# Performance work log

Hardware: AMD Instinct MI355X
Metric: run time of the kernel (lower is better)

The kernel has to match this reference:

```python
import jax, jax.numpy as jnp
import numpy as np

B, L, D0, H, K = 16, 256, 64, 128, 512  # batch, seq, feat, hidden, codebook size


def _p(key, shape, scale=0.05):
    return jax.random.normal(key, shape, jnp.float32) * scale


def setup_inputs() -> dict:
    key = jax.random.key(0)
    ks = jax.random.split(key, 32)
    inp = {
        "inputs": jax.random.normal(ks[0], (B, L, D0), jnp.float32),
        "input_lens": jnp.full((B,), L, dtype=jnp.int64),
        "in_mask": jnp.ones((B, L), jnp.float32),
        # encoder params
        "enc_lin1_W": _p(ks[1], (H, D0)), "enc_lin1_b": jnp.zeros((H,), jnp.float32),
        "enc_Wih_f": _p(ks[2], (4 * H, H)), "enc_Whh_f": _p(ks[3], (4 * H, H)), "enc_b_f": jnp.zeros((4 * H,), jnp.float32),
        "enc_Wih_b": _p(ks[4], (4 * H, H)), "enc_Whh_b": _p(ks[5], (4 * H, H)), "enc_b_b": jnp.zeros((4 * H,), jnp.float32),
        "enc_lin2_W": _p(ks[6], (H, 2 * H)), "enc_lin2_b": jnp.zeros((H,), jnp.float32),
        # VQ codebook (K codes of dim H), init uniform(-1/K, 1/K) as in torch
        "vq_emb": jax.random.uniform(ks[7], (K, H), jnp.float32, -1.0 / K, 1.0 / K),
        # decoder params
        "dec_lin1_W": _p(ks[8], (H, D0)), "dec_lin1_b": jnp.zeros((H,), jnp.float32),
        "dec_Wih": _p(ks[9], (4 * H, H)), "dec_Whh": _p(ks[10], (4 * H, H)), "dec_b": jnp.zeros((4 * H,), jnp.float32),
        "attn_Wq": _p(ks[11], (H, H)), "attn_bq": jnp.zeros((H,), jnp.float32),
        "attn_Wk": _p(ks[12], (H, H)), "attn_bk": jnp.zeros((H,), jnp.float32),
        "attn_Wv": _p(ks[13], (H, H)), "attn_bv": jnp.zeros((H,), jnp.float32),
        "dec_lin2_W": _p(ks[14], (D0, H)), "dec_lin2_b": jnp.zeros((D0,), jnp.float32),
    }
    return inp


def _lstm_cell(x, h, c, Wih, Whh, b):
    g = x @ Wih.T + h @ Whh.T + b  # (B, 4H)
    i, f, gg, o = jnp.split(g, 4, axis=-1)
    c = jax.nn.sigmoid(f) * c + jax.nn.sigmoid(i) * jnp.tanh(gg)
    h = jax.nn.sigmoid(o) * jnp.tanh(c)
    return h, c


def _lstm_scan(x_blh, Wih, Whh, b, reverse=False):
    Bb = x_blh.shape[0]
    Hh = Whh.shape[1]
    init = (jnp.zeros((Bb, Hh), x_blh.dtype), jnp.zeros((Bb, Hh), x_blh.dtype))

    def step(carry, x):
        h, c = _lstm_cell(x, carry[0], carry[1], Wih, Whh, b)
        return (h, c), h

    _, hs = jax.lax.scan(step, init, jnp.swapaxes(x_blh, 0, 1), reverse=reverse)
    return jnp.swapaxes(hs, 0, 1)  # (B, L, H)


def _forward(inputs, in_mask, p):
    # ---- encoder: Linear -> ReLU -> BiLSTM -> Linear (full-length sequences) ----
    enc_x = jax.nn.relu(inputs @ p["enc_lin1_W"].T + p["enc_lin1_b"])
    hf = _lstm_scan(enc_x, p["enc_Wih_f"], p["enc_Whh_f"], p["enc_b_f"], reverse=False)
    hb = _lstm_scan(enc_x, p["enc_Wih_b"], p["enc_Whh_b"], p["enc_b_b"], reverse=True)
    ze = jnp.concatenate([hf, hb], axis=-1) @ p["enc_lin2_W"].T + p["enc_lin2_b"]  # (B,L,H)

    # ---- VQ: nearest codebook entry (expanded ||a-b||^2, avoids (B,L,K,C) tensor) ----
    emb = p["vq_emb"]  # (K, H)
    dist = (jnp.sum(ze * ze, -1, keepdims=True)
            - 2.0 * jnp.einsum("blc,kc->blk", ze, emb)
            + jnp.sum(emb * emb, -1)[None, None, :])  # (B,L,K)
    nearest = jnp.argmin(dist, axis=-1)  # (B,L) int
    zq = emb[nearest]  # (B,L,H)
    dec_in = ze + jax.lax.stop_gradient(zq - ze)  # straight-through

    k_proj = dec_in @ p["attn_Wk"].T + p["attn_bk"]  # (B,L,H)
    v_proj = dec_in @ p["attn_Wv"].T + p["attn_bv"]
    scale = 1.0 / jnp.sqrt(jnp.float32(H))
    mask_add = jnp.where(in_mask == 0, -1e9, 0.0).astype(jnp.float32)  # (B,L)

    def dec_step(carry, _):
        h, c, tok = carry
        x = jax.nn.relu(tok @ p["dec_lin1_W"].T + p["dec_lin1_b"])  # (B,H)
        h, c = _lstm_cell(x, h, c, p["dec_Wih"], p["dec_Whh"], p["dec_b"])
        q = h @ p["attn_Wq"].T + p["attn_bq"]  # (B,H)
        scores = jnp.einsum("bd,bld->bl", q, k_proj) * scale + mask_add
        attn = jax.nn.softmax(scores, axis=-1)  # (B,L)
        ctx = jnp.einsum("bl,bld->bd", attn, v_proj)  # (B,H)
        out = ctx @ p["dec_lin2_W"].T + p["dec_lin2_b"]  # (B,D0)
        return (h, c, out), (out, attn)

    Bb = inputs.shape[0]
    init = (jnp.zeros((Bb, H), jnp.float32), jnp.zeros((Bb, H), jnp.float32), jnp.zeros((Bb, D0), jnp.float32))
    _, (outs, attns) = jax.lax.scan(dec_step, init, None, length=dec_in.shape[1])
    dec_out = jnp.swapaxes(outs, 0, 1)  # (B,L,D0)
    attn_w = jnp.swapaxes(attns, 0, 1)  # (B,L,L)
    return dec_out, attn_w, ze, zq


def reference(inputs, input_lens, in_mask, enc_lin1_W, enc_lin1_b, enc_Wih_f, enc_Whh_f, enc_b_f,
              enc_Wih_b, enc_Whh_b, enc_b_b, enc_lin2_W, enc_lin2_b, vq_emb,
              dec_lin1_W, dec_lin1_b, dec_Wih, dec_Whh, dec_b,
              attn_Wq, attn_bq, attn_Wk, attn_bk, attn_Wv, attn_bv, dec_lin2_W, dec_lin2_b):
    p = dict(enc_lin1_W=enc_lin1_W, enc_lin1_b=enc_lin1_b, enc_Wih_f=enc_Wih_f, enc_Whh_f=enc_Whh_f,
             enc_b_f=enc_b_f, enc_Wih_b=enc_Wih_b, enc_Whh_b=enc_Whh_b, enc_b_b=enc_b_b,
             enc_lin2_W=enc_lin2_W, enc_lin2_b=enc_lin2_b, vq_emb=vq_emb,
             dec_lin1_W=dec_lin1_W, dec_lin1_b=dec_lin1_b, dec_Wih=dec_Wih, dec_Whh=dec_Whh, dec_b=dec_b,
             attn_Wq=attn_Wq, attn_bq=attn_bq, attn_Wk=attn_Wk, attn_bk=attn_bk,
             attn_Wv=attn_Wv, attn_bv=attn_bv, dec_lin2_W=dec_lin2_W, dec_lin2_b=dec_lin2_b)
    return _forward(inputs, in_mask, p)
```

## Files before the change

kernel.cpp:

```cpp
#include <hip/hip_runtime.h>

#define Bn  16
#define Ln  256
#define D0n 64
#define Hn  128
#define H4n 512
#define Kn  512
#define BLn 4096

typedef float f4 __attribute__((ext_vector_type(4)));
typedef unsigned long long u64;

__device__ __forceinline__ float sigf(float x) { return 1.0f / (1.0f + expf(-x)); }

__device__ __forceinline__ float fma4v(f4 w, f4 x, float acc) {
    acc = fmaf(w.x, x.x, acc);
    acc = fmaf(w.y, x.y, acc);
    acc = fmaf(w.z, x.z, acc);
    acc = fmaf(w.w, x.w, acc);
    return acc;
}

__device__ __forceinline__ float dotn(const f4* __restrict__ a,
                                      const f4* __restrict__ w, int n4) {
    float a0 = 0.f, a1 = 0.f, a2 = 0.f, a3 = 0.f;
    for (int i = 0; i < n4; i += 4) {
        a0 = fma4v(a[i], w[i], a0);
        a1 = fma4v(a[i + 1], w[i + 1], a1);
        a2 = fma4v(a[i + 2], w[i + 2], a2);
        a3 = fma4v(a[i + 3], w[i + 3], a3);
    }
    return (a0 + a1) + (a2 + a3);
}

__device__ __forceinline__ void tag_store(u64* p, float v, unsigned tag) {
    u64 pk = ((u64)tag << 32) | (u64)__float_as_uint(v);
    __hip_atomic_store(p, pk, __ATOMIC_RELAXED, __HIP_MEMORY_SCOPE_AGENT);
}
__device__ __forceinline__ float tag_poll(u64* p, unsigned tag) {
    u64 v;
    do {
        v = __hip_atomic_load(p, __ATOMIC_RELAXED, __HIP_MEMORY_SCOPE_AGENT);
    } while ((unsigned)(v >> 32) != tag);
    return __uint_as_float((unsigned)v);
}

__global__ __launch_bounds__(256)
void k_gemm(const float* __restrict__ X, const float* __restrict__ W,
            const float* __restrict__ b, float* __restrict__ Y,
            int K, int out_dim, int do_relu, float scale) {
    __shared__ __align__(16) f4 wt4[4096];
    const int K4 = K >> 2;
    const int tid = threadIdx.x;
    const int c = tid & 63, rpart = tid >> 6;
    const f4* W4 = (const f4*)W;
    const int per = K4 >> 2;
    for (int j = 0; j < per; ++j) {
        int col = rpart * per + j;
        wt4[col * 64 + c] = W4[(size_t)(blockIdx.x * 64 + c) * K4 + col];
    }
    __syncthreads();
    const f4* X4 = (const f4*)X;
    const float bc = b ? b[blockIdx.x * 64 + c] : 0.f;
    const int cidx = blockIdx.x * 64 + c;
    for (int i = 0; i < 4; ++i) {
        int rbase = blockIdx.y * 64 + i * 16 + rpart * 4;
        const f4* xr0 = X4 + (size_t)(rbase + 0) * K4;
        const f4* xr1 = X4 + (size_t)(rbase + 1) * K4;
        const f4* xr2 = X4 + (size_t)(rbase + 2) * K4;
        const f4* xr3 = X4 + (size_t)(rbase + 3) * K4;
        float a0 = 0.f, a1 = 0.f, a2 = 0.f, a3 = 0.f;
        for (int k4 = 0; k4 < K4; ++k4) {
            f4 wv = wt4[k4 * 64 + c];
            a0 = fma4v(wv, xr0[k4], a0);
            a1 = fma4v(wv, xr1[k4], a1);
            a2 = fma4v(wv, xr2[k4], a2);
            a3 = fma4v(wv, xr3[k4], a3);
        }
        a0 = scale * a0 + bc; a1 = scale * a1 + bc;
        a2 = scale * a2 + bc; a3 = scale * a3 + bc;
        if (do_relu) {
            a0 = fmaxf(a0, 0.f); a1 = fmaxf(a1, 0.f);
            a2 = fmaxf(a2, 0.f); a3 = fmaxf(a3, 0.f);
        }
        Y[(size_t)(rbase + 0) * out_dim + cidx] = a0;
        Y[(size_t)(rbase + 1) * out_dim + cidx] = a1;
        Y[(size_t)(rbase + 2) * out_dim + cidx] = a2;
        Y[(size_t)(rbase + 3) * out_dim + cidx] = a3;
    }
}

__global__ __launch_bounds__(256)
void k_gemm2(const float* __restrict__ X,
             const float* __restrict__ Wf, const float* __restrict__ bf,
             float* __restrict__ Yf,
             const float* __restrict__ Wb, const float* __restrict__ bb,
             float* __restrict__ Yb, int K, int out_dim) {
    __shared__ __align__(16) f4 wt4[4096];
    const float* W = blockIdx.z ? Wb : Wf;
    const float* bb_ = blockIdx.z ? bb : bf;
    float* Y = blockIdx.z ? Yb : Yf;
    const int K4 = K >> 2;
    const int tid = threadIdx.x;
    const int c = tid & 63, rpart = tid >> 6;
    const f4* W4 = (const f4*)W;
    const int per = K4 >> 2;
    for (int j = 0; j < per; ++j) {
        int col = rpart * per + j;
        wt4[col * 64 + c] = W4[(size_t)(blockIdx.x * 64 + c) * K4 + col];
    }
    __syncthreads();
    const f4* X4 = (const f4*)X;
    const float bc = bb_[blockIdx.x * 64 + c];
    const int cidx = blockIdx.x * 64 + c;
    for (int i = 0; i < 4; ++i) {
        int rbase = blockIdx.y * 64 + i * 16 + rpart * 4;
        const f4* xr0 = X4 + (size_t)(rbase + 0) * K4;
        const f4* xr1 = X4 + (size_t)(rbase + 1) * K4;
        const f4* xr2 = X4 + (size_t)(rbase + 2) * K4;
        const f4* xr3 = X4 + (size_t)(rbase + 3) * K4;
        float a0 = 0.f, a1 = 0.f, a2 = 0.f, a3 = 0.f;
        for (int k4 = 0; k4 < K4; ++k4) {
            f4 wv = wt4[k4 * 64 + c];
            a0 = fma4v(wv, xr0[k4], a0);
            a1 = fma4v(wv, xr1[k4], a1);
            a2 = fma4v(wv, xr2[k4], a2);
            a3 = fma4v(wv, xr3[k4], a3);
        }
        Y[(size_t)(rbase + 0) * out_dim + cidx] = a0 + bc;
        Y[(size_t)(rbase + 1) * out_dim + cidx] = a1 + bc;
        Y[(size_t)(rbase + 2) * out_dim + cidx] = a2 + bc;
        Y[(size_t)(rbase + 3) * out_dim + cidx] = a3 + bc;
    }
}

#define SCL 0.088388347648318447f

__global__ void k_prep(const float* __restrict__ Wq, const float* __restrict__ Wk,
                       const float* __restrict__ Wv, const float* __restrict__ W2,
                       const float* __restrict__ bk, const float* __restrict__ bv,
                       const float* __restrict__ b2, const float* __restrict__ bq,
                       float* __restrict__ Wcat, float* __restrict__ bcat,
                       float* __restrict__ u, float* __restrict__ ub,
                       const f4* __restrict__ dec_Wih, f4* __restrict__ WihL,
                       const f4* __restrict__ whf, const f4* __restrict__ whb,
                       f4* __restrict__ WhhL,
                       const float* __restrict__ emb, float* __restrict__ c2,
                       int* __restrict__ zbuf) {
    const int blk = blockIdx.x, tid = threadIdx.x;
    if (blk < 64) {
        int idx = blk * 256 + tid;
        int c = idx >> 7, d = idx & 127;
        float acc = 0.f;
        for (int r = 0; r < Hn; ++r)
            acc = fmaf(Wq[(size_t)r * Hn + c], Wk[(size_t)r * Hn + d], acc);
        Wcat[(size_t)c * Hn + d] = SCL * acc;
    } else if (blk < 96) {
        int idx = (blk - 64) * 256 + tid;
        int o = idx >> 7, d = idx & 127;
        float acc = 0.f;
        for (int r = 0; r < Hn; ++r)
            acc = fmaf(W2[(size_t)o * Hn + r], Wv[(size_t)r * Hn + d], acc);
        Wcat[(size_t)(128 + o) * Hn + d] = acc;
    } else if (blk < 160) {
        int idx = (blk - 96) * 256 + tid;
        int t = idx & 511, side = (idx >> 9) & 1, k = idx >> 10;
        int rl = t >> 1;
        int grow = (rl >> 6) * 128 + side * 64 + (rl & 63);
        WihL[idx] = dec_Wih[(size_t)grow * 32 + (t & 1) * 16 + k];
    } else if (blk < 224) {
        int idx = (blk - 160) * 256 + tid;
        int row = idx & 511, k = (idx >> 9) & 15, dir = idx >> 13;
        const f4* src = dir ? whb : whf;
        WhhL[idx] = src[(size_t)row * 32 + 16 + k];
    } else if (blk == 224) {
        if (tid < 128) {
            float acc = 0.f;
            for (int r = 0; r < Hn; ++r)
                acc = fmaf(Wq[(size_t)r * Hn + tid], bk[r], acc);
            bcat[tid] = SCL * acc;
        } else if (tid < 192) {
            int o = tid - 128;
            float acc = b2[o];
            for (int r = 0; r < Hn; ++r)
                acc = fmaf(W2[(size_t)o * Hn + r], bv[r], acc);
            bcat[tid] = acc;
        }
    } else if (blk == 225) {
        if (tid < 128) {
            float acc = 0.f;
            for (int r = 0; r < Hn; ++r)
                acc = fmaf(bq[r], Wk[(size_t)r * Hn + tid], acc);
            u[tid] = SCL * acc;
        } else if (tid == 128) {
            float acc = 0.f;
            for (int r = 0; r < Hn; ++r) acc = fmaf(bq[r], bk[r], acc);
            ub[0] = SCL * acc;
        }
    } else if (blk < 228) {
        int k = (blk - 226) * 256 + tid;
        if (k < Kn) {
            const f4* e4 = (const f4*)(emb + (size_t)k * Hn);
            float acc = 0.f;
            for (int i = 0; i < Hn / 4; ++i) {
                f4 v = e4[i];
                acc = fmaf(v.x, v.x, acc); acc = fmaf(v.y, v.y, acc);
                acc = fmaf(v.z, v.z, acc); acc = fmaf(v.w, v.w, acc);
            }
            c2[k] = acc;
        }
    } else {
        int idx = (blk - 228) * 256 + tid;
        if (idx < 8192) zbuf[idx] = 0;
    }
}

__global__ void k_rearrKQF(const f4* __restrict__ in, f4* __restrict__ out) {
    int idx = blockIdx.x * blockDim.x + threadIdx.x;
    if (idx >= 131072) return;
    int tid = idx & 511, k = (idx >> 9) & 15, b = idx >> 13;
    out[idx] = in[((size_t)b * 256 + (tid >> 1)) * 48 + (tid & 1) * 16 + k];
}

__global__ void k_cst(const float* __restrict__ zq, const float* __restrict__ u,
                      const float* __restrict__ ub, const float* __restrict__ mask,
                      float* __restrict__ cst) {
    int p = blockIdx.x * blockDim.x + threadIdx.x;
    if (p >= BLn) return;
    float a = dotn((const f4*)u, (const f4*)(zq + (size_t)p * Hn), Hn >> 2);
    cst[p] = a + ub[0] + (mask[p] == 0.f ? -1e9f : 0.f);
}

__global__ __launch_bounds__(128)
void k_vqpick(const float* __restrict__ dist, const float* __restrict__ emb,
              float* __restrict__ zq) {
    const int p = blockIdx.x, tid = threadIdx.x;
    __shared__ int best_s;
    if (tid < 64) {
        float best = 3.0e38f; int bi = 0;
        for (int j = 0; j < 8; ++j) {
            int k = j * 64 + tid;
            float d = dist[(size_t)p * Kn + k];
            if (d < best) { best = d; bi = k; }
        }
        for (int off = 32; off > 0; off >>= 1) {
            float ov = __shfl_xor(best, off);
            int   oi = __shfl_xor(bi, off);
            if (ov < best || (ov == best && oi < bi)) { best = ov; bi = oi; }
        }
        if (tid == 0) best_s = bi;
    }
    __syncthreads();
    zq[(size_t)p * Hn + tid] = emb[(size_t)best_s * Hn + tid];
}

__global__ __launch_bounds__(512, 1)
void k_lstm3(const float* __restrict__ xWf, const float* __restrict__ xWb,
             const float* __restrict__ Whh_f, const float* __restrict__ Whh_b,
             const float* __restrict__ WhhL_g, float* __restrict__ hcat) {
    const int b   = blockIdx.x & 15;
    const int dir = blockIdx.x >> 4;
    const int tid = threadIdx.x;
    const float* xW  = dir ? xWb : xWf;
    const f4* Whh4   = (const f4*)(dir ? Whh_b : Whh_f);

    __shared__ __align__(16) f4 wh2_s[16 * 512];
    __shared__ __align__(16) float h_s[Hn];
    __shared__ float g_s[H4n];

    f4 w[16];
#pragma unroll
    for (int f = 0; f < 16; ++f) w[f] = Whh4[(size_t)tid * 32 + f];
#pragma unroll
    for (int f = 0; f < 16; ++f) asm volatile("" : "+v"(w[f]));

    const f4* WhhL4 = (const f4*)WhhL_g;
#pragma unroll
    for (int k = 0; k < 16; ++k)
        wh2_s[k * 512 + tid] = WhhL4[(size_t)dir * 8192 + k * 512 + tid];

    float c_reg = 0.f;
    if (tid < Hn) h_s[tid] = 0.f;

    const int t0 = dir ? (Ln - 1) : 0;
    float xw_v = xW[((size_t)b * Ln + t0) * H4n + tid];
    __syncthreads();

    for (int s = 0; s < Ln; ++s) {
        const int t = dir ? (Ln - 1 - s) : s;
        float xw_n = 0.f;
        if (s + 1 < Ln) {
            int tn = dir ? (Ln - 2 - s) : (s + 1);
            xw_n = xW[((size_t)b * Ln + tn) * H4n + tid];
        }
        {
            const f4* h4 = (const f4*)h_s;
            float a0 = 0.f, a1 = 0.f, a2 = 0.f, a3 = 0.f;
#pragma unroll
            for (int f = 0; f < 16; f += 4) {
                a0 = fma4v(w[f],     h4[f],     a0);
                a1 = fma4v(w[f + 1], h4[f + 1], a1);
                a2 = fma4v(w[f + 2], h4[f + 2], a2);
                a3 = fma4v(w[f + 3], h4[f + 3], a3);
            }
#pragma unroll
            for (int f = 0; f < 16; f += 4) {
                a0 = fma4v(wh2_s[f * 512 + tid],       h4[16 + f],     a0);
                a1 = fma4v(wh2_s[(f + 1) * 512 + tid], h4[16 + f + 1], a1);
                a2 = fma4v(wh2_s[(f + 2) * 512 + tid], h4[16 + f + 2], a2);
                a3 = fma4v(wh2_s[(f + 3) * 512 + tid], h4[16 + f + 3], a3);
            }
            g_s[tid] = (a0 + a1) + (a2 + a3) + xw_v;
        }
        __syncthreads();
        if (tid < Hn) {
            float ig = sigf(g_s[tid]);
            float fg = sigf(g_s[Hn + tid]);
            float gg = tanhf(g_s[2 * Hn + tid]);
            float og = sigf(g_s[3 * Hn + tid]);
            c_reg = fg * c_reg + ig * gg;
            float hv = og * tanhf(c_reg);
            h_s[tid] = hv;
            hcat[((size_t)b * Ln + t) * (2 * Hn) + dir * Hn + tid] = hv;
        }
        __syncthreads();
        xw_v = xw_n;
    }
}

__global__ __launch_bounds__(512, 1)
void k_decoder(const float* __restrict__ kqF_g, const float* __restrict__ ycat_g,
               const float* __restrict__ cst_g,
               const float* __restrict__ W1,  const float* __restrict__ b1_g,
               const float* __restrict__ WihL_g, const float* __restrict__ Whh,
               const float* __restrict__ bd_g, u64* gxd,
               float* __restrict__ dec_out, float* __restrict__ attn_w) {
    const int b    = blockIdx.x & 15;
    const int side = blockIdx.x >> 4;
    const int tid  = threadIdx.x;

    __shared__ __align__(16) f4 wih_s[16 * 512];
    __shared__ __align__(16) float tok_s[D0n];
    __shared__ __align__(16) float x_s[Hn];
    __shared__ __align__(16) float h_s[Hn];
    __shared__ float g_loc[256];
    __shared__ float s_s[Ln];
    __shared__ float attn_sp[8][33];
    __shared__ float cst_s[Ln];
    __shared__ float b1_s[Hn];

    const int rl = tid >> 1, ghalf = tid & 1;
    const int grow = (rl >> 6) * 128 + side * 64 + (rl & 63);

    const f4* Whh4 = (const f4*)Whh;
    f4 whh[16];
#pragma unroll
    for (int f = 0; f < 16; ++f) whh[f] = Whh4[(size_t)grow * 32 + ghalf * 16 + f];
    float bdr = bd_g[grow];
    const int o = tid >> 3, slab = tid & 7;
    float vwr[32];
#pragma unroll
    for (int l = 0; l < 32; ++l)
        vwr[l] = ycat_g[((size_t)b * Ln + slab * 32 + l) * 192 + 128 + o];
#pragma unroll
    for (int f = 0; f < 16; ++f) asm volatile("" : "+v"(whh[f]));
#pragma unroll
    for (int l = 0; l < 32; ++l) asm volatile("" : "+v"(vwr[l]));
    asm volatile("" : "+v"(bdr));

    const f4* WihL4 = (const f4*)WihL_g;
#pragma unroll
    for (int k = 0; k < 16; ++k)
        wih_s[k * 512 + tid] = WihL4[(size_t)k * 1024 + side * 512 + tid];
    if (tid < D0n) tok_s[tid] = 0.f;
    if (tid < Hn)  { h_s[tid] = 0.f; b1_s[tid] = b1_g[tid]; }
    if (tid < Ln)  cst_s[tid] = cst_g[(size_t)b * Ln + tid];
    float c_reg = 0.f;
    __syncthreads();

    u64* gx_mine = gxd + (b * 2 + side) * 128;
    u64* gx_peer = gxd + (b * 2 + (side ^ 1)) * 128;

    const int ar = tid >> 2, ap = tid & 3;
    const f4* W1_4 = (const f4*)W1;
    const f4* kqF  = (const f4*)kqF_g + (size_t)b * 8192;
    const int dbase = (tid & 1) * 16;

    for (int t = 0; t < Ln; ++t) {
        {
            const f4* t4 = (const f4*)tok_s;
            float u0 = 0.f, u1 = 0.f;
#pragma unroll
            for (int k = 0; k < 4; k += 2) {
                f4 wa  = W1_4[(size_t)ar * 16 + ap * 4 + k];
                f4 wb2 = W1_4[(size_t)ar * 16 + ap * 4 + k + 1];
                u0 = fma4v(wa,  t4[ap * 4 + k],     u0);
                u1 = fma4v(wb2, t4[ap * 4 + k + 1], u1);
            }
            float a = u0 + u1;
            a += __shfl_xor(a, 1);
            a += __shfl_xor(a, 2);
            if (ap == 0) x_s[ar] = fmaxf(a + b1_s[ar], 0.f);
        }
        __syncthreads();
        {
            const f4* x4 = (const f4*)x_s + ghalf * 16;
            const f4* h4 = (const f4*)h_s + ghalf * 16;
            float a0 = 0.f, a1 = 0.f, a2 = 0.f, a3 = 0.f;
#pragma unroll
            for (int f = 0; f < 16; f += 4) {
                a0 = fma4v(wih_s[f * 512 + tid],       x4[f],     a0);
                a1 = fma4v(wih_s[(f + 1) * 512 + tid], x4[f + 1], a1);
                a2 = fma4v(wih_s[(f + 2) * 512 + tid], x4[f + 2], a2);
                a3 = fma4v(wih_s[(f + 3) * 512 + tid], x4[f + 3], a3);
            }
#pragma unroll
            for (int f = 0; f < 16; f += 4) {
                a0 = fma4v(whh[f],     h4[f],     a0);
                a1 = fma4v(whh[f + 1], h4[f + 1], a1);
                a2 = fma4v(whh[f + 2], h4[f + 2], a2);
                a3 = fma4v(whh[f + 3], h4[f + 3], a3);
            }
            float a = (a0 + a1) + (a2 + a3);
            a += __shfl_xor(a, 1);
            if (ghalf == 0) g_loc[rl] = a + bdr;
        }
        __syncthreads();
        if (tid < 64) {
            float ig = sigf(g_loc[tid]);
            float fg = sigf(g_loc[64 + tid]);
            float gg = tanhf(g_loc[128 + tid]);
            float og = sigf(g_loc[192 + tid]);
            c_reg = fg * c_reg + ig * gg;
            float hv = og * tanhf(c_reg);
            h_s[side * 64 + tid] = hv;
            tag_store(&gx_mine[(t & 1) * 64 + tid], hv, (unsigned)(t + 1));
            h_s[(side ^ 1) * 64 + tid] =
                tag_poll(&gx_peer[(t & 1) * 64 + tid], (unsigned)(t + 1));
        }
        __syncthreads();
        {
            const f4* h4 = (const f4*)h_s;
            float a0 = 0.f, a1 = 0.f;
#pragma unroll
            for (int k = 0; k < 16; k += 2) {
                f4 q0 = kqF[(size_t)k * 512 + tid];
                f4 q1 = kqF[(size_t)(k + 1) * 512 + tid];
                a0 = fma4v(q0, h4[dbase + k],     a0);
                a1 = fma4v(q1, h4[dbase + k + 1], a1);
            }
            float a = a0 + a1;
            a += __shfl_xor(a, 1);
            if ((tid & 1) == 0) s_s[tid >> 1] = a + cst_s[tid >> 1];
        }
        __syncthreads();
        if (tid < 64) {
            float v0 = s_s[tid],       v1 = s_s[tid + 64];
            float v2 = s_s[tid + 128], v3 = s_s[tid + 192];
            float m = fmaxf(fmaxf(v0, v1), fmaxf(v2, v3));
#pragma unroll
            for (int o2 = 32; o2 > 0; o2 >>= 1) m = fmaxf(m, __shfl_xor(m, o2));
            float e0 = expf(v0 - m), e1 = expf(v1 - m);
            float e2 = expf(v2 - m), e3 = expf(v3 - m);
            float ss = (e0 + e1) + (e2 + e3);
#pragma unroll
            for (int o2 = 32; o2 > 0; o2 >>= 1) ss += __shfl_xor(ss, o2);
            float inv = 1.f / ss;
            e0 *= inv; e1 *= inv; e2 *= inv; e3 *= inv;
            attn_sp[tid >> 5][tid & 31] = e0;
            attn_sp[(tid + 64) >> 5][tid & 31] = e1;
            attn_sp[(tid + 128) >> 5][tid & 31] = e2;
            attn_sp[(tid + 192) >> 5][tid & 31] = e3;
            if (side == 0) {
                float* aw = attn_w + ((size_t)b * Ln + t) * Ln;
                aw[tid] = e0; aw[tid + 64] = e1;
                aw[tid + 128] = e2; aw[tid + 192] = e3;
            }
        }
        __syncthreads();
        {
            const float* as = attn_sp[slab];
            float g0 = 0.f, g1 = 0.f, g2 = 0.f, g3 = 0.f;
#pragma unroll
            for (int l = 0; l < 32; l += 4) {
                g0 = fmaf(as[l],     vwr[l],     g0);
                g1 = fmaf(as[l + 1], vwr[l + 1], g1);
                g2 = fmaf(as[l + 2], vwr[l + 2], g2);
                g3 = fmaf(as[l + 3], vwr[l + 3], g3);
            }
            float a = (g0 + g1) + (g2 + g3);
            a += __shfl_xor(a, 1);
            a += __shfl_xor(a, 2);
            a += __shfl_xor(a, 4);
            if (slab == 0) {
                tok_s[o] = a;
                if (side == 1) dec_out[((size_t)b * Ln + t) * D0n + o] = a;
            }
        }
        __syncthreads();
    }
}

extern "C" void kernel_launch(void* const* d_in, const int* in_sizes, int n_in,
                              void* d_out, int out_size, void* d_ws, size_t ws_size,
                              hipStream_t stream) {
    const float* inputs     = (const float*)d_in[0];
    const float* in_mask    = (const float*)d_in[2];
    const float* enc_lin1_W = (const float*)d_in[3];
    const float* enc_lin1_b = (const float*)d_in[4];
    const float* enc_Wih_f  = (const float*)d_in[5];
    const float* enc_Whh_f  = (const float*)d_in[6];
    const float* enc_b_f    = (const float*)d_in[7];
    const float* enc_Wih_b  = (const float*)d_in[8];
    const float* enc_Whh_b  = (const float*)d_in[9];
    const float* enc_b_b    = (const float*)d_in[10];
    const float* enc_lin2_W = (const float*)d_in[11];
    const float* enc_lin2_b = (const float*)d_in[12];
    const float* vq_emb     = (const float*)d_in[13];
    const float* dec_lin1_W = (const float*)d_in[14];
    const float* dec_lin1_b = (const float*)d_in[15];
    const float* dec_Wih    = (const float*)d_in[16];
    const float* dec_Whh    = (const float*)d_in[17];
    const float* dec_b      = (const float*)d_in[18];
    const float* attn_Wq    = (const float*)d_in[19];
    const float* attn_bq    = (const float*)d_in[20];
    const float* attn_Wk    = (const float*)d_in[21];
    const float* attn_bk    = (const float*)d_in[22];
    const float* attn_Wv    = (const float*)d_in[23];
    const float* attn_bv    = (const float*)d_in[24];
    const float* dec_lin2_W = (const float*)d_in[25];
    const float* dec_lin2_b = (const float*)d_in[26];

    float* out     = (float*)d_out;
    float* dec_out = out;
    float* attn_w  = out + 262144;
    float* ze      = out + 1310720;
    float* zq      = out + 1835008;

    float* ws    = (float*)d_ws;
    float* enc_x = ws;
    float* xWf   = enc_x + 524288;
    float* xWb   = xWf + 2097152;
    float* hcat  = xWb + 2097152;
    float* base2 = hcat + 1048576;
    float* c2    = base2;
    u64*   gxd   = (u64*)(base2 + 512);
    float* Wcat  = base2 + 512 + 8192;
    float* bcat  = Wcat + 24576;
    float* uvec  = bcat + 256;
    float* ubv   = uvec + 128;
    float* WihL  = ubv + 16;
    float* WhhL  = WihL + 65536;
    float* dist  = xWf;
    float* KQF   = xWf;
    float* Ycat  = xWb;
    float* cst   = xWb + 786432;

    dim3 blk(256);
    k_prep<<<260, 256, 0, stream>>>(attn_Wq, attn_Wk, attn_Wv, dec_lin2_W,
                                    attn_bk, attn_bv, dec_lin2_b, attn_bq,
                                    Wcat, bcat, uvec, ubv,
                                    (const f4*)dec_Wih, (f4*)WihL,
                                    (const f4*)enc_Whh_f, (const f4*)enc_Whh_b,
                                    (f4*)WhhL, vq_emb, c2, (int*)gxd);
    k_gemm<<<dim3(2, 64), blk, 0, stream>>>(inputs, enc_lin1_W, enc_lin1_b, enc_x, D0n, Hn, 1, 1.f);
    k_gemm2<<<dim3(8, 64, 2), blk, 0, stream>>>(enc_x,
                                                enc_Wih_f, enc_b_f, xWf,
                                                enc_Wih_b, enc_b_b, xWb, Hn, H4n);
    k_lstm3<<<32, 512, 0, stream>>>(xWf, xWb, enc_Whh_f, enc_Whh_b, WhhL, hcat);
    k_gemm<<<dim3(2, 64), blk, 0, stream>>>(hcat, enc_lin2_W, enc_lin2_b, ze, 2 * Hn, Hn, 0, 1.f);
    k_gemm<<<dim3(8, 64), blk, 0, stream>>>(ze, vq_emb, c2, dist, Hn, Kn, 0, -2.f);
    k_vqpick<<<BLn, 128, 0, stream>>>(dist, vq_emb, zq);
    k_gemm<<<dim3(3, 64), blk, 0, stream>>>(zq, Wcat, bcat, Ycat, Hn, 192, 0, 1.f);
    k_cst<<<Bn, 256, 0, stream>>>(zq, uvec, ubv, in_mask, cst);
    k_rearrKQF<<<512, 256, 0, stream>>>((const f4*)Ycat, (f4*)KQF);
    k_decoder<<<32, 512, 0, stream>>>(KQF, Ycat, cst,
                                      dec_lin1_W, dec_lin1_b,
                                      WihL, dec_Whh, dec_b, gxd,
                                      dec_out, attn_w);
}
```

Before: 1.590 ms.

## Remap encoder LSTM gate rows so each wavefront owns full gate quads, drop barrier

Reassigns gate rows to threads so each 64-lane wavefront holds the i/f/g/o rows for 16 hidden units, with the pinned and LDS-staged Whh slices remapped to match in the prep kernel. Gate values are exchanged with wavefront shuffles instead of a shared g buffer, which removes one __syncthreads per timestep from the 256-step serial recurrence. In exchange, only a quarter of the lanes in each wave do the cell update, and the shuffles add cross-lane traffic.

```diff
diff --git a/kernel.cpp b/kernel.cpp
--- a/kernel.cpp
+++ b/kernel.cpp
@@ -170,9 +170,10 @@
         WihL[idx] = dec_Wih[(size_t)grow * 32 + (t & 1) * 16 + k];
     } else if (blk < 224) {
         int idx = (blk - 160) * 256 + tid;
-        int row = idx & 511, k = (idx >> 9) & 15, dir = idx >> 13;
+        int t = idx & 511, k = (idx >> 9) & 15, dir = idx >> 13;
+        int grow = ((t & 63) >> 4) * 128 + (t >> 6) * 16 + (t & 15);
         const f4* src = dir ? whb : whf;
-        WhhL[idx] = src[(size_t)row * 32 + 16 + k];
+        WhhL[idx] = src[(size_t)grow * 32 + 16 + k];
     } else if (blk == 224) {
         if (tid < 128) {
             float acc = 0.f;
@@ -255,24 +256,26 @@
 }
 
 __global__ __launch_bounds__(512, 1)
-void k_lstm3(const float* __restrict__ xWf, const float* __restrict__ xWb,
+void k_lstm4(const float* __restrict__ xWf, const float* __restrict__ xWb,
              const float* __restrict__ Whh_f, const float* __restrict__ Whh_b,
              const float* __restrict__ WhhL_g, float* __restrict__ hcat) {
     const int b   = blockIdx.x & 15;
     const int dir = blockIdx.x >> 4;
     const int tid = threadIdx.x;
+    const int w   = tid >> 6, lane = tid & 63;
+    const int q   = lane >> 4, j = lane & 15;
+    const int grow = q * 128 + w * 16 + j;
     const float* xW  = dir ? xWb : xWf;
     const f4* Whh4   = (const f4*)(dir ? Whh_b : Whh_f);
 
     __shared__ __align__(16) f4 wh2_s[16 * 512];
     __shared__ __align__(16) float h_s[Hn];
-    __shared__ float g_s[H4n];
-
-    f4 w[16];
-#pragma unroll
-    for (int f = 0; f < 16; ++f) w[f] = Whh4[(size_t)tid * 32 + f];
-#pragma unroll
-    for (int f = 0; f < 16; ++f) asm volatile("" : "+v"(w[f]));
+
+    f4 wpin[16];
+#pragma unroll
+    for (int f = 0; f < 16; ++f) wpin[f] = Whh4[(size_t)grow * 32 + f];
+#pragma unroll
+    for (int f = 0; f < 16; ++f) asm volatile("" : "+v"(wpin[f]));
 
     const f4* WhhL4 = (const f4*)WhhL_g;
 #pragma unroll
@@ -283,7 +286,7 @@
     if (tid < Hn) h_s[tid] = 0.f;
 
     const int t0 = dir ? (Ln - 1) : 0;
-    float xw_v = xW[((size_t)b * Ln + t0) * H4n + tid];
+    float xw_v = xW[((size_t)b * Ln + t0) * H4n + grow];
     __syncthreads();
 
     for (int s = 0; s < Ln; ++s) {
@@ -291,17 +294,18 @@
         float xw_n = 0.f;
         if (s + 1 < Ln) {
             int tn = dir ? (Ln - 2 - s) : (s + 1);
-            xw_n = xW[((size_t)b * Ln + tn) * H4n + tid];
-        }
+            xw_n = xW[((size_t)b * Ln + tn) * H4n + grow];
+        }
+        float g;
         {
             const f4* h4 = (const f4*)h_s;
             float a0 = 0.f, a1 = 0.f, a2 = 0.f, a3 = 0.f;
 #pragma unroll
             for (int f = 0; f < 16; f += 4) {
-                a0 = fma4v(w[f],     h4[f],     a0);
-                a1 = fma4v(w[f + 1], h4[f + 1], a1);
-                a2 = fma4v(w[f + 2], h4[f + 2], a2);
-                a3 = fma4v(w[f + 3], h4[f + 3], a3);
+                a0 = fma4v(wpin[f],     h4[f],     a0);
+                a1 = fma4v(wpin[f + 1], h4[f + 1], a1);
+                a2 = fma4v(wpin[f + 2], h4[f + 2], a2);
+                a3 = fma4v(wpin[f + 3], h4[f + 3], a3);
             }
 #pragma unroll
             for (int f = 0; f < 16; f += 4) {
@@ -310,18 +314,20 @@
                 a2 = fma4v(wh2_s[(f + 2) * 512 + tid], h4[16 + f + 2], a2);
                 a3 = fma4v(wh2_s[(f + 3) * 512 + tid], h4[16 + f + 3], a3);
             }
-            g_s[tid] = (a0 + a1) + (a2 + a3) + xw_v;
-        }
-        __syncthreads();
-        if (tid < Hn) {
-            float ig = sigf(g_s[tid]);
-            float fg = sigf(g_s[Hn + tid]);
-            float gg = tanhf(g_s[2 * Hn + tid]);
-            float og = sigf(g_s[3 * Hn + tid]);
+            g = (a0 + a1) + (a2 + a3) + xw_v;
+        }
+        float gI = __shfl(g, j);
+        float gF = __shfl(g, 16 + j);
+        float gG = __shfl(g, 32 + j);
+        float gO = __shfl(g, 48 + j);
+        if (q == 0) {
+            float ig = sigf(gI), fg = sigf(gF);
+            float gg = tanhf(gG), og = sigf(gO);
             c_reg = fg * c_reg + ig * gg;
             float hv = og * tanhf(c_reg);
-            h_s[tid] = hv;
-            hcat[((size_t)b * Ln + t) * (2 * Hn) + dir * Hn + tid] = hv;
+            int cc = w * 16 + j;
+            h_s[cc] = hv;
+            hcat[((size_t)b * Ln + t) * (2 * Hn) + dir * Hn + cc] = hv;
         }
         __syncthreads();
         xw_v = xw_n;
@@ -567,7 +573,7 @@
     k_gemm2<<<dim3(8, 64, 2), blk, 0, stream>>>(enc_x,
                                                 enc_Wih_f, enc_b_f, xWf,
                                                 enc_Wih_b, enc_b_b, xWb, Hn, H4n);
-    k_lstm3<<<32, 512, 0, stream>>>(xWf, xWb, enc_Whh_f, enc_Whh_b, WhhL, hcat);
+    k_lstm4<<<32, 512, 0, stream>>>(xWf, xWb, enc_Whh_f, enc_Whh_b, WhhL, hcat);
     k_gemm<<<dim3(2, 64), blk, 0, stream>>>(hcat, enc_lin2_W, enc_lin2_b, ze, 2 * Hn, Hn, 0, 1.f);
     k_gemm<<<dim3(8, 64), blk, 0, stream>>>(ze, vq_emb, c2, dist, Hn, Kn, 0, -2.f);
     k_vqpick<<<BLn, 128, 0, stream>>>(dist, vq_emb, zq);
```

Result: faster. 1.543 ms (median of 2 runs) (-3.0%).
